# Optimization experiments

Hardware: AMD Instinct MI355X
Metric: run time of the kernel (lower is better)

The kernel has to match this reference:

```python
import jax, jax.numpy as jnp
import numpy as np

# Static diagonal offsets of the SparseDIA matrix (eqx static field).
OFFSETS = (-128, -64, -8, -1, 0, 1, 8, 64, 128)
N = 8192   # matrix dimension (diags.shape[1])
M = 4096   # number of dense columns in `other`


def setup_inputs() -> dict:
    key = jax.random.key(0)
    k1, k2 = jax.random.split(key)
    diags = jax.random.normal(k1, (len(OFFSETS), N), dtype=jnp.float32)
    other = jax.random.normal(k2, (N, M), dtype=jnp.float32)
    return {"diags": diags, "other": other}


def reference(diags, other):
    """SparseDIA._matmul_dense(left_matmul=True): out = A_dia @ other.

    For each static offset k, rows [top:bottom] of the output accumulate
    diag[start:end] (the valid part of the stored diagonal) times the
    matching rows of `other`. Offsets are Python ints, so all slices are
    static and jit-compatible.
    """
    n = other.shape[0]
    out = jnp.zeros_like(other)
    for k, offset in enumerate(OFFSETS):
        start = max(0, offset)
        end = min(n, n + offset)
        top = max(0, -offset)
        bottom = top + (end - start)
        out = out.at[top:bottom, :].add(
            diags[k, start:end, None] * other[start:end, :]
        )
    return out
```

## Files before the change

### kernel.cpp

```cpp
#include <hip/hip_runtime.h>


#define DIA_N   8192
#define DIA_M   4096
#define M4      (DIA_M / 4)
#define CB      8
#define BR      256
#define HALO    128
#define RING    768
#define NB      16
#define GROUP   (BR * NB)
#define THREADS 1024
#define NWAVES  (THREADS / 64)
#define RT      (BR / (THREADS / 8))

typedef float f4 __attribute__((ext_vector_type(4)));
typedef __attribute__((address_space(3))) unsigned int       lds_uint;
typedef const __attribute__((address_space(1))) unsigned int glb_uint;

__global__ __launch_bounds__(THREADS) void sparse_dia_kernel(
    const float* __restrict__ diags,
    const float* __restrict__ other,
    float* __restrict__ out)
{
    constexpr int OFF[9] = {-128, -64, -8, -1, 0, 1, 8, 64, 128};

    __shared__ f4    ring[RING][CB];
    __shared__ float dlds[2][9 * BR];

    const int tid  = threadIdx.x;
    const int gr0  = blockIdx.y * GROUP;
    const int cb4  = blockIdx.x * CB;

    const int wave = tid >> 6;
    const int lane = tid & 63;
    const int lrow = lane >> 3;
    const int lcol = lane & 7;

    auto stage_ring = [&](int slot0, int q0, int ninst) {
#pragma unroll
        for (int s = 0; s < 4; ++s) {
            if (s >= ninst) break;
            const int inst = wave * ninst + s;
            int q = q0 + inst * 8 + lrow;
            q = (q < 0) ? 0 : (q >= DIA_N ? DIA_N - 1 : q);
            const float* src = other + ((size_t)q * DIA_M + (size_t)(cb4 + lcol) * 4);
            __builtin_amdgcn_global_load_lds(
                (glb_uint*)src,
                (lds_uint*)&ring[slot0 + inst * 8][0],
                16, 0, 0);
        }
    };

    auto stage_diag = [&](int buf, int t) {
        const int bs = gr0 + t * BR;
#pragma unroll
        for (int f = tid; f < 9 * BR; f += THREADS) {
            const int k = f >> 8;
            const int i = f & (BR - 1);
            const int q  = bs + i + OFF[k];
            const int qc = (q < 0) ? 0 : (q >= DIA_N ? DIA_N - 1 : q);
            float v = diags[k * DIA_N + qc];
            v = ((unsigned)q < (unsigned)DIA_N) ? v : 0.f;
            dlds[buf][f] = v;
        }
    };

    f4* __restrict__ out4 = (f4*)out;

    stage_ring(0, gr0 - HALO, (2 * BR / 8) / NWAVES);
    stage_diag(0, 0);
    __syncthreads();

    const int c  = tid & 7;
    const int i0 = (tid >> 3) * RT;

    for (int t = 0; t < NB; ++t) {
        if (t + 1 < NB) {
            const int u = 2 * BR + t * BR;
            stage_ring(u % RING, gr0 - HALO + u, (BR / 8) / NWAVES);
            stage_diag((t + 1) & 1, t + 1);
        }

        const int buf  = t & 1;
        const int base = (HALO + t * BR) % RING;
        auto slot = [&](int x) { int s = base + x; return (s >= RING) ? s - RING : s; };

        f4 vm = ring[slot(i0 - 1)][c];
        f4 v0 = ring[slot(i0    )][c];
        f4 vp = ring[slot(i0 + 1)][c];

#pragma unroll
        for (int j = 0; j < RT; ++j) {
            const int i = i0 + j;
            float dk[9];
#pragma unroll
            for (int k = 0; k < 9; ++k) dk[k] = dlds[buf][k * BR + i];

            f4 a = dk[4] * v0;
            a += dk[3] * vm;
            a += dk[5] * vp;
            a += dk[2] * ring[slot(i - 8)][c];
            a += dk[6] * ring[slot(i + 8)][c];
            a += dk[0] * ring[slot(i - 128)][c];
            a += dk[1] * ring[slot(i - 64)][c];
            a += dk[7] * ring[slot(i + 64)][c];
            a += dk[8] * ring[slot(i + 128)][c];

            out4[(size_t)(gr0 + t * BR + i) * M4 + cb4 + c] = a;

            vm = v0; v0 = vp;
            if (j < RT - 1) vp = ring[slot(i + 2)][c];
        }

        __syncthreads();
    }
}

extern "C" void kernel_launch(void* const* d_in, const int* in_sizes, int n_in,
                              void* d_out, int out_size, void* d_ws, size_t ws_size,
                              hipStream_t stream) {
    const float* diags = (const float*)d_in[0];
    const float* other = (const float*)d_in[1];
    float* out         = (float*)d_out;

    dim3 block(THREADS, 1, 1);
    dim3 grid(M4 / CB, DIA_N / GROUP, 1);
    sparse_dia_kernel<<<grid, block, 0, stream>>>(diags, other, out);
}
```

Baseline: 246.2 us.

## Halve row block, swizzle LDS ring columns, one output row per thread

The per-iteration row block drops from 256 to 128 and the LDS ring from 768 to 512 slots, so ring indexing becomes a power-of-two mask. GROUP shrinks to 2048 rows, which doubles the number of blocks in the grid. Each thread now computes exactly one output row and reads all nine neighbour rows from LDS, replacing the previous two-row sliding register window. Global-to-LDS loads place column chunks with an XOR swizzle (lcol ^ lrow) to avoid LDS bank conflicts, and launch bounds add a min-blocks hint of 8. Less LDS per block and more blocks may raise occupancy, but each thread does more LDS reads per output and the per-block halo overhead grows relative to useful rows.

```diff
diff --git a/kernel.cpp b/kernel.cpp
--- a/kernel.cpp
+++ b/kernel.cpp
@@ -5,20 +5,19 @@
 #define DIA_M   4096
 #define M4      (DIA_M / 4)
 #define CB      8
-#define BR      256
+#define BR      128
 #define HALO    128
-#define RING    768
+#define RING    512
 #define NB      16
 #define GROUP   (BR * NB)
 #define THREADS 1024
 #define NWAVES  (THREADS / 64)
-#define RT      (BR / (THREADS / 8))
 
 typedef float f4 __attribute__((ext_vector_type(4)));
 typedef __attribute__((address_space(3))) unsigned int       lds_uint;
 typedef const __attribute__((address_space(1))) unsigned int glb_uint;
 
-__global__ __launch_bounds__(THREADS) void sparse_dia_kernel(
+__global__ __launch_bounds__(THREADS, 8) void sparse_dia_kernel(
     const float* __restrict__ diags,
     const float* __restrict__ other,
     float* __restrict__ out)
@@ -36,15 +35,16 @@
     const int lane = tid & 63;
     const int lrow = lane >> 3;
     const int lcol = lane & 7;
+    const int scol = lcol ^ lrow;
 
     auto stage_ring = [&](int slot0, int q0, int ninst) {
 #pragma unroll
-        for (int s = 0; s < 4; ++s) {
+        for (int s = 0; s < 3; ++s) {
             if (s >= ninst) break;
             const int inst = wave * ninst + s;
             int q = q0 + inst * 8 + lrow;
             q = (q < 0) ? 0 : (q >= DIA_N ? DIA_N - 1 : q);
-            const float* src = other + ((size_t)q * DIA_M + (size_t)(cb4 + lcol) * 4);
+            const float* src = other + ((size_t)q * DIA_M + (size_t)(cb4 + scol) * 4);
             __builtin_amdgcn_global_load_lds(
                 (glb_uint*)src,
                 (lds_uint*)&ring[slot0 + inst * 8][0],
@@ -54,10 +54,9 @@
 
     auto stage_diag = [&](int buf, int t) {
         const int bs = gr0 + t * BR;
-#pragma unroll
         for (int f = tid; f < 9 * BR; f += THREADS) {
-            const int k = f >> 8;
-            const int i = f & (BR - 1);
+            const int k  = f >> 7;
+            const int i  = f & (BR - 1);
             const int q  = bs + i + OFF[k];
             const int qc = (q < 0) ? 0 : (q >= DIA_N ? DIA_N - 1 : q);
             float v = diags[k * DIA_N + qc];
@@ -68,50 +67,35 @@
 
     f4* __restrict__ out4 = (f4*)out;
 
-    stage_ring(0, gr0 - HALO, (2 * BR / 8) / NWAVES);
+    stage_ring(0, gr0 - HALO, 3);
     stage_diag(0, 0);
     __syncthreads();
 
-    const int c  = tid & 7;
-    const int i0 = (tid >> 3) * RT;
+    const int c = tid & 7;
+    const int i = tid >> 3;
 
     for (int t = 0; t < NB; ++t) {
         if (t + 1 < NB) {
-            const int u = 2 * BR + t * BR;
-            stage_ring(u % RING, gr0 - HALO + u, (BR / 8) / NWAVES);
+            const int u = (BR + 2 * HALO) + t * BR;
+            stage_ring(u & (RING - 1), gr0 - HALO + u, 1);
             stage_diag((t + 1) & 1, t + 1);
         }
 
         const int buf  = t & 1;
-        const int base = (HALO + t * BR) % RING;
-        auto slot = [&](int x) { int s = base + x; return (s >= RING) ? s - RING : s; };
+        const int base = (HALO + t * BR) & (RING - 1);
 
-        f4 vm = ring[slot(i0 - 1)][c];
-        f4 v0 = ring[slot(i0    )][c];
-        f4 vp = ring[slot(i0 + 1)][c];
+        float dk[9];
+#pragma unroll
+        for (int k = 0; k < 9; ++k) dk[k] = dlds[buf][k * BR + i];
 
+        f4 a = (f4){0.f, 0.f, 0.f, 0.f};
 #pragma unroll
-        for (int j = 0; j < RT; ++j) {
-            const int i = i0 + j;
-            float dk[9];
-#pragma unroll
-            for (int k = 0; k < 9; ++k) dk[k] = dlds[buf][k * BR + i];
+        for (int k = 0; k < 9; ++k) {
+            const int slot = (base + i + OFF[k]) & (RING - 1);
+            a += dk[k] * ring[slot][c ^ (slot & 7)];
+        }
 
-            f4 a = dk[4] * v0;
-            a += dk[3] * vm;
-            a += dk[5] * vp;
-            a += dk[2] * ring[slot(i - 8)][c];
-            a += dk[6] * ring[slot(i + 8)][c];
-            a += dk[0] * ring[slot(i - 128)][c];
-            a += dk[1] * ring[slot(i - 64)][c];
-            a += dk[7] * ring[slot(i + 64)][c];
-            a += dk[8] * ring[slot(i + 128)][c];
-
-            out4[(size_t)(gr0 + t * BR + i) * M4 + cb4 + c] = a;
-
-            vm = v0; v0 = vp;
-            if (j < RT - 1) vp = ring[slot(i + 2)][c];
-        }
+        out4[(size_t)(gr0 + t * BR + i) * M4 + cb4 + c] = a;
 
         __syncthreads();
     }
```

Result: no change. 244.4 us (-0.7%).
